# Kernel tuning notes

Hardware: AMD Instinct MI355X
Metric: run time of the kernel (lower is better)

The kernel has to match this reference:

```python
import jax, jax.numpy as jnp
import numpy as np

B, N_PER, E_PER = 100, 1000, 12000  # graphs, nodes/graph, edges/graph
N, E = B * N_PER, B * E_PER
K = int(np.ceil(0.8 * N_PER))  # TopKPooling ratio=0.8 -> 800 kept nodes/graph


def setup_inputs() -> dict:
    key = jax.random.key(0)
    ks = jax.random.split(key, 16)
    g = jnp.repeat(jnp.arange(B, dtype=jnp.int64), E_PER)
    src = g * N_PER + jax.random.randint(ks[0], (E,), 0, N_PER)
    dst = g * N_PER + jax.random.randint(ks[1], (E,), 0, N_PER)
    edge_index = jnp.stack([src, dst]).astype(jnp.int64)
    edge_attr = jax.random.uniform(ks[2], (E,), dtype=jnp.float32) + 0.1  # positive edge weights
    x = jax.random.normal(ks[3], (N, 3), dtype=jnp.float32)
    batch = jnp.repeat(jnp.arange(B, dtype=jnp.int64), N_PER)
    s = 0.1
    return {
        'x': x, 'edge_index': edge_index, 'edge_attr': edge_attr, 'batch': batch,
        'conv1_w': jax.random.normal(ks[4], (3, 64), dtype=jnp.float32) * s,
        'conv1_b': jnp.zeros((64,), dtype=jnp.float32),
        'conv2_w': jax.random.normal(ks[5], (64, 64), dtype=jnp.float32) * s,
        'conv2_b': jnp.zeros((64,), dtype=jnp.float32),
        'pool_w': jax.random.normal(ks[6], (64,), dtype=jnp.float32) * s,
        'lin1_w': jax.random.normal(ks[7], (64, 64), dtype=jnp.float32) * s,
        'lin1_b': jnp.zeros((64,), dtype=jnp.float32),
        'lin2_w': jax.random.normal(ks[8], (64, 32), dtype=jnp.float32) * s,
        'lin2_b': jnp.zeros((32,), dtype=jnp.float32),
        'lin3_w': jax.random.normal(ks[9], (32, 1), dtype=jnp.float32) * s,
        'lin3_b': jnp.zeros((1,), dtype=jnp.float32),
    }


def gcn_conv(x, row, col, ew, W, b):
    # PyG GCNConv with edge_weight and implicit self-loops (weight 1):
    # deg[i] = sum_{e: col=i} ew[e] + 1;  norm_e = d^{-1/2}[row]*ew*d^{-1/2}[col]
    h = x @ W  # [N, out]
    deg = jax.ops.segment_sum(ew, col, num_segments=N) + 1.0
    dinv = jax.lax.rsqrt(deg)
    msg = (dinv[row] * ew * dinv[col])[:, None] * h[row]  # [E, out]
    out = jax.ops.segment_sum(msg, col, num_segments=N)
    out = out + (dinv * dinv)[:, None] * h  # self-loop term
    return out + b


def reference(x, edge_index, edge_attr, batch, conv1_w, conv1_b, conv2_w, conv2_b,
              pool_w, lin1_w, lin1_b, lin2_w, lin2_b, lin3_w, lin3_b):
    row, col = edge_index[0], edge_index[1]
    h = jax.nn.relu(gcn_conv(x, row, col, edge_attr, conv1_w, conv1_b))
    x1 = h.reshape(B, N_PER, 64).mean(axis=1)  # global_mean_pool (equal-size graphs)
    h = jax.nn.relu(gcn_conv(h, row, col, edge_attr, conv2_w, conv2_b))
    # TopKPooling: score = tanh(x.w / ||w||), keep top-K per graph, gate by score
    score = jnp.tanh(h @ pool_w / jnp.linalg.norm(pool_w))  # [N]
    score_bn = score.reshape(B, N_PER)
    vals, idx = jax.lax.top_k(score_bn, K)  # [B, K]
    h_bn = h.reshape(B, N_PER, 64)
    h_sel = jnp.take_along_axis(h_bn, idx[..., None], axis=1) * vals[..., None]
    x2 = h_sel.mean(axis=1)  # global_mean_pool on pooled graph
    z = x1 + x2
    z = jax.nn.relu(z @ lin1_w + lin1_b)
    z = jax.nn.relu(z @ lin2_w + lin2_b)  # dropout is identity in eval mode
    out = jax.nn.sigmoid(z @ lin3_w + lin3_b)[:, 0]
    return out
```

## Files before the change

kernel.cpp:

```cpp
#include <hip/hip_runtime.h>

#define B_G   100
#define N_PER 1000
#define E_PER 12000
#define NTOT  (B_G * N_PER)
#define ETOT  (B_G * E_PER)
#define KSEL  800
#define EPT   12

typedef __attribute__((ext_vector_type(8))) short short8;
typedef __attribute__((ext_vector_type(4))) float float4_;

__device__ __forceinline__ unsigned short f2bf(float f) {
    unsigned u = __float_as_uint(f);
    u += 0x7fffu + ((u >> 16) & 1u);
    return (unsigned short)(u >> 16);
}
__device__ __forceinline__ float upk(unsigned q) {
    return __uint_as_float(q & 0xFFFF0000u);
}
__device__ __forceinline__ float dec_raw(unsigned byte7f) {
    return __uint_as_float(byte7f << 20);
}
__device__ __forceinline__ unsigned enc_fp8(float z) {
    unsigned u = __float_as_uint(z * 0x1p-120f);
    u += 0x7FFFFu + ((u >> 20) & 1u);
    return u >> 20;
}

#define CONV2_TI(TI, AF0, AF1) do {                                            \
    const int t_ = wid + (TI) * 16;                                            \
    const int li_ = t_ * 16 + nloc;                                            \
    const bool valid_ = li_ < N_PER;                                           \
    float acc_[16];                                                            \
    int s_ = 0, cn_ = 0;                                                       \
    if (valid_) {                                                              \
        uint4 rv_ = *(const uint4*)(zs + li_ * 64 + ((kgrp ^ ((li_ >> 1) & 3)) << 4)); \
        _Pragma("unroll")                                                      \
        for (int j = 0; j < 4; j++) {                                          \
            acc_[j]      = dec_raw((rv_.x >> (8 * j)) & 0x7Fu);                \
            acc_[4 + j]  = dec_raw((rv_.y >> (8 * j)) & 0x7Fu);                \
            acc_[8 + j]  = dec_raw((rv_.z >> (8 * j)) & 0x7Fu);                \
            acc_[12 + j] = dec_raw((rv_.w >> (8 * j)) & 0x7Fu);                \
        }                                                                      \
        s_ = li_ ? ends[li_ - 1] : 0;                                          \
        cn_ = ends[li_] - s_;                                                  \
    } else {                                                                   \
        _Pragma("unroll")                                                      \
        for (int j = 0; j < 16; j++) acc_[j] = 0.f;                            \
    }                                                                          \
    int mx_ = cn_;                                                             \
    _Pragma("unroll")                                                          \
    for (int m = 1; m < 16; m <<= 1) mx_ = max(mx_, __shfl_xor(mx_, m));       \
    for (int k = 0; k < mx_; k++) {                                            \
        if (k < cn_) {                                                         \
            unsigned q_ = csr[s_ + k];                                         \
            int src_ = (int)(q_ & 0xFFFFu);                                    \
            float wv_ = upk(q_);                                               \
            uint4 rv_ = *(const uint4*)(zs + src_ * 64 + ((kgrp ^ ((src_ >> 1) & 3)) << 4)); \
            _Pragma("unroll")                                                  \
            for (int j = 0; j < 4; j++) {                                      \
                acc_[j]      += wv_ * dec_raw((rv_.x >> (8 * j)) & 0x7Fu);     \
                acc_[4 + j]  += wv_ * dec_raw((rv_.y >> (8 * j)) & 0x7Fu);     \
                acc_[8 + j]  += wv_ * dec_raw((rv_.z >> (8 * j)) & 0x7Fu);     \
                acc_[12 + j] += wv_ * dec_raw((rv_.w >> (8 * j)) & 0x7Fu);     \
            }                                                                  \
        }                                                                      \
    }                                                                          \
    float scale_ = (valid_ ? dl[li_] : 0.f) * 0x1p120f;                        \
    _Pragma("unroll")                                                          \
    for (int j = 0; j < 8; j++) {                                              \
        AF0[j] = (short)f2bf(scale_ * acc_[j]);                                \
        AF1[j] = (short)f2bf(scale_ * acc_[8 + j]);                            \
    }                                                                          \
} while (0)

#define W2_TI(TI, AF0, AF1) do {                                               \
    const int t_ = wid + (TI) * 16;                                            \
    if (t_ < 63) {                                                             \
        float4_ accv_[4];                                                      \
        _Pragma("unroll")                                                      \
        for (int c = 0; c < 4; ++c) accv_[c] = (float4_){0.f, 0.f, 0.f, 0.f};  \
        _Pragma("unroll")                                                      \
        for (int c = 0; c < 4; ++c) {                                          \
            accv_[c] = __builtin_amdgcn_mfma_f32_16x16x32_bf16(AF0, Bf[0][c], accv_[c], 0, 0, 0); \
            accv_[c] = __builtin_amdgcn_mfma_f32_16x16x32_bf16(AF1, Bf[1][c], accv_[c], 0, 0, 0); \
        }                                                                      \
        _Pragma("unroll")                                                      \
        for (int r2 = 0; r2 < 4; ++r2) {                                       \
            int li2_ = t_ * 16 + kgrp * 4 + r2;                                \
            bool valid2_ = li2_ < N_PER;                                       \
            float sp_ = 0.f;                                                   \
            _Pragma("unroll")                                                  \
            for (int c = 0; c < 4; ++c) {                                      \
                float hv_ = fmaxf(accv_[c][r2] + b2c[c], 0.f);                 \
                sp_ += hv_ * pwc[c];                                           \
                if (valid2_) zs[li2_ * 64 + c * 16 + nloc] = (unsigned char)enc_fp8(hv_); \
            }                                                                  \
            _Pragma("unroll")                                                  \
            for (int m = 1; m < 16; m <<= 1) sp_ += __shfl_xor(sp_, m);        \
            if (valid2_ && nloc == 0) {                                        \
                float scv_ = tanhf(sp_ * invn);                                \
                unsigned bits_ = __float_as_uint(scv_);                        \
                unsigned u_ = (bits_ & 0x80000000u) ? ~bits_ : (bits_ | 0x80000000u); \
                keys[li2_] = ((unsigned long long)u_ << 32) | (unsigned)(1023 - li2_); \
            }                                                                  \
        }                                                                      \
    }                                                                          \
} while (0)

__global__ __launch_bounds__(1024)
__attribute__((amdgpu_waves_per_eu(4, 4))) void k_all(
    const int* __restrict__ ei, const float* __restrict__ ew,
    const float* __restrict__ x,
    const float* __restrict__ w1, const float* __restrict__ b1,
    const float* __restrict__ w2, const float* __restrict__ b2,
    const float* __restrict__ pw,
    const float* __restrict__ l1w, const float* __restrict__ l1b,
    const float* __restrict__ l2w, const float* __restrict__ l2b,
    const float* __restrict__ l3w, const float* __restrict__ l3b,
    float* __restrict__ out) {
    __shared__ __align__(16) unsigned char smem[136832];
    unsigned char* zs = smem;
    float* xl = (float*)smem;
    unsigned* csr = (unsigned*)(smem + 64000);
    int*   ends = (int*)(smem + 112000);
    float* dl   = (float*)(smem + 116096);
    int*   posc = (int*)(smem + 116096);
    int*   wpart = (int*)(smem + 120192);
    float* x1b   = (float*)(smem + 120192);
    unsigned char* uA = smem + 120448;
    float* aggv = (float*)uA;

    int b = blockIdx.x, tid = threadIdx.x;
    int wid = tid >> 6, lane = tid & 63;
    int gbase = b * N_PER, ebase = b * E_PER;

    int esrc[EPT], edst[EPT]; float eww[EPT];
    int ne = (tid < (E_PER - (EPT - 1) * 1024)) ? EPT : EPT - 1;
#pragma unroll
    for (int i = 0; i < EPT; i++) {
        if (i < ne) {
            int e = tid + i * 1024;
            esrc[i] = ei[ebase + e] - gbase;
            edst[i] = ei[ETOT + ebase + e] - gbase;
            eww[i]  = ew[ebase + e];
        }
    }
    ends[tid] = 0;
    for (int i = tid; i < N_PER * 3; i += 1024) xl[i] = x[(size_t)gbase * 3 + i];
    __syncthreads();
#pragma unroll
    for (int i = 0; i < EPT; i++)
        if (i < ne) atomicAdd(&ends[edst[i]], 1);
    __syncthreads();
    int v = ends[tid];
    int sc = v;
#pragma unroll
    for (int m = 1; m < 64; m <<= 1) {
        int t = __shfl_up(sc, m);
        if (lane >= m) sc += t;
    }
    if (lane == 63) wpart[wid] = sc;
    __syncthreads();
    if (tid < 16) {
        int s2 = wpart[tid];
#pragma unroll
        for (int m = 1; m < 16; m <<= 1) {
            int t = __shfl_up(s2, m);
            if (tid >= m) s2 += t;
        }
        wpart[tid] = s2;
    }
    __syncthreads();
    int incl = sc + (wid > 0 ? wpart[wid - 1] : 0);
    ends[tid] = incl;
    posc[tid] = incl - v;
    __syncthreads();
#pragma unroll
    for (int i = 0; i < EPT; i++)
        if (i < ne) {
            int p = atomicAdd(&posc[edst[i]], 1);
            csr[p] = ((unsigned)f2bf(eww[i]) << 16) | (unsigned)esrc[i];
        }
    __syncthreads();
    float dmy = 0.f;
    int s0i = 0, e0i = 0;
    if (tid < N_PER) {
        s0i = tid ? ends[tid - 1] : 0;
        e0i = ends[tid];
        float s0 = 0.f, s1 = 0.f;
        int k = s0i;
        for (; k + 2 <= e0i; k += 2) { s0 += upk(csr[k]); s1 += upk(csr[k + 1]); }
        if (k < e0i) s0 += upk(csr[k]);
        dmy = rsqrtf(s0 + s1 + 1.0f);
        dl[tid] = dmy;
        xl[tid * 3 + 0] *= dmy;
        xl[tid * 3 + 1] *= dmy;
        xl[tid * 3 + 2] *= dmy;
    }
    __syncthreads();
    if (tid < N_PER) {
        float a0 = xl[tid * 3 + 0], a1 = xl[tid * 3 + 1], a2 = xl[tid * 3 + 2];
        for (int k = s0i; k < e0i; k++) {
            unsigned q = csr[k];
            int i0 = (int)(q & 0xFFFFu) * 3;
            float wv = upk(q);
            a0 += wv * xl[i0]; a1 += wv * xl[i0 + 1]; a2 += wv * xl[i0 + 2];
        }
        aggv[tid * 3 + 0] = dmy * a0;
        aggv[tid * 3 + 1] = dmy * a1;
        aggv[tid * 3 + 2] = dmy * a2;
    }
    __syncthreads();
    {
        float w0 = w1[lane], w1v = w1[64 + lane], w2v = w1[128 + lane], bf = b1[lane];
        float* sred = (float*)(uA + 12288);
        float px = 0.f;
        int chunk = (lane & 31) >> 3;
        int word  = ((lane >= 32) ? 2 : 0) + ((lane & 7) >> 2);
        for (int node = wid; node < N_PER; node += 16) {
            float a0 = aggv[node * 3], a1 = aggv[node * 3 + 1], a2 = aggv[node * 3 + 2];
            float hv = fmaxf(a0 * w0 + a1 * w1v + a2 * w2v + bf, 0.f);
            px += hv;
            unsigned byte = enc_fp8(dl[node] * hv);
            unsigned t1 = __shfl_xor(byte, 1);
            unsigned v16 = (lane & 1) ? (t1 | (byte << 8)) : (byte | (t1 << 8));
            unsigned t2 = __shfl_xor(v16, 2);
            unsigned v32 = (lane & 2) ? (t2 | (v16 << 16)) : (v16 | (t2 << 16));
            if ((lane & 3) == 0) {
                int cs = chunk ^ ((node >> 1) & 3);
                *(unsigned*)(zs + node * 64 + cs * 16 + word * 4) = v32;
            }
        }
        sred[wid * 64 + lane] = px;
        __syncthreads();
        if (tid < 64) {
            float t = 0.f;
            for (int r = 0; r < 16; r++) t += sred[r * 64 + tid];
            x1b[tid] = t * (1.0f / N_PER);
        }
    }
    int kgrp = lane >> 4, nloc = lane & 15;
    short8 Af0a, Af0b, Af1a, Af1b, Af2a, Af2b, Af3a, Af3b;
    CONV2_TI(0, Af0a, Af0b);
    CONV2_TI(1, Af1a, Af1b);
    CONV2_TI(2, Af2a, Af2b);
    CONV2_TI(3, Af3a, Af3b);
    __syncthreads();
    unsigned long long* keys = (unsigned long long*)uA;
    {
        short8 Bf[2][4];
#pragma unroll
        for (int kh = 0; kh < 2; ++kh)
#pragma unroll
            for (int c = 0; c < 4; ++c) {
                short8 t;
#pragma unroll
                for (int j = 0; j < 8; ++j)
                    t[j] = (short)f2bf(w2[(kh * 32 + kgrp * 8 + j) * 64 + c * 16 + nloc]);
                Bf[kh][c] = t;
            }
        float b2c[4], pwc[4];
#pragma unroll
        for (int c = 0; c < 4; ++c) {
            b2c[c] = b2[c * 16 + nloc];
            pwc[c] = pw[c * 16 + nloc];
        }
        float invn;
        {
            float p = pw[lane], pn = p * p;
#pragma unroll
            for (int m = 32; m; m >>= 1) pn += __shfl_xor(pn, m);
            invn = rsqrtf(pn);
        }
        if (tid >= N_PER) keys[tid] = 0ull;
        W2_TI(0, Af0a, Af0b);
        W2_TI(1, Af1a, Af1b);
        W2_TI(2, Af2a, Af2b);
        W2_TI(3, Af3a, Af3b);
    }
    __syncthreads();
    {
        unsigned long long key = keys[tid];
        for (int k = 2; k <= 1024; k <<= 1) {
            for (int j = k >> 1; j > 0; j >>= 1) {
                bool desc = (tid & k) == 0;
                unsigned long long p;
                if (j >= 64) {
                    keys[tid] = key;
                    __syncthreads();
                    p = keys[tid ^ j];
                    __syncthreads();
                } else {
                    p = __shfl_xor(key, j);
                }
                bool low = (tid & j) == 0;
                bool sw = low ? (desc ? (key < p) : (key > p))
                              : (desc ? (p < key) : (p > key));
                if (sw) key = p;
            }
        }
        keys[tid] = key;
    }
    __syncthreads();
    float* red   = (float*)(uA + 8192);
    float* a1buf = (float*)(uA + 12288);
    float* a2buf = (float*)(uA + 12544);
    float* zbuf  = (float*)(uA + 12672);
    {
        int f = tid & 63, w16 = tid >> 6;
        float acc2 = 0.f;
        for (int r = w16; r < KSEL; r += 16) {
            unsigned long long key = keys[r];
            int idx = 1023 - (int)(key & 0xFFFFFFFFu);
            unsigned u = (unsigned)(key >> 32);
            unsigned bits = (u & 0x80000000u) ? (u & 0x7FFFFFFFu) : ~u;
            float valS = __uint_as_float(bits) * 0x1p120f;
            acc2 += valS * dec_raw((unsigned)zs[idx * 64 + f] & 0x7Fu);
        }
        red[tid] = acc2;
    }
    __syncthreads();
    if (tid < 64) {
        float s2 = 0.f;
        for (int ww = 0; ww < 16; ww++) s2 += red[ww * 64 + tid];
        zbuf[tid] = x1b[tid] + s2 * (1.0f / KSEL);
    }
    __syncthreads();
    if (tid < 64) {
        float a = l1b[tid];
        for (int k = 0; k < 64; k++) a += zbuf[k] * l1w[k * 64 + tid];
        a1buf[tid] = fmaxf(a, 0.f);
    }
    __syncthreads();
    if (tid < 32) {
        float a = l2b[tid];
        for (int k = 0; k < 64; k++) a += a1buf[k] * l2w[k * 32 + tid];
        a2buf[tid] = fmaxf(a, 0.f);
    }
    __syncthreads();
    if (tid == 0) {
        float t = l3b[0];
        for (int k = 0; k < 32; k++) t += a2buf[k] * l3w[k];
        out[b] = 1.0f / (1.0f + expf(-t));
    }
}

extern "C" void kernel_launch(void* const* d_in, const int* in_sizes, int n_in,
                              void* d_out, int out_size, void* d_ws, size_t ws_size,
                              hipStream_t stream) {
    const float* x   = (const float*)d_in[0];
    const int*   ei  = (const int*)d_in[1];
    const float* ew  = (const float*)d_in[2];
    const float* c1w = (const float*)d_in[4];
    const float* c1b = (const float*)d_in[5];
    const float* c2w = (const float*)d_in[6];
    const float* c2b = (const float*)d_in[7];
    const float* pw  = (const float*)d_in[8];
    const float* l1w = (const float*)d_in[9];
    const float* l1b = (const float*)d_in[10];
    const float* l2w = (const float*)d_in[11];
    const float* l2b = (const float*)d_in[12];
    const float* l3w = (const float*)d_in[13];
    const float* l3b = (const float*)d_in[14];
    float* out = (float*)d_out;
    (void)d_ws; (void)ws_size; (void)in_sizes; (void)n_in; (void)out_size;

    k_all<<<B_G, 1024, 0, stream>>>(ei, ew, x, c1w, c1b, c2w, c2b, pw,
                                    l1w, l1b, l2w, l2b, l3w, l3b, out);
}
```

Measured before the change: 181.3 us.

## Split each graph across two cooperating blocks with flag handoff for conv2

Launches two blocks per graph. Each block redundantly builds the CSR and runs conv1, then computes half of the conv2 row tiles. The second block copies its half of the fp8 features and score keys to workspace and sets a release flag. The first block spin-waits on that flag, copies the data back in, and runs the sort and MLP tail. This doubles the block count from 100 to 200 to fill more CUs, at the cost of duplicated front-end work, a global-memory exchange, and a spin-wait that relies on both blocks being co-resident.

```diff
diff --git a/kernel.cpp b/kernel.cpp
--- a/kernel.cpp
+++ b/kernel.cpp
@@ -109,138 +109,236 @@
     }                                                                          \
 } while (0)
 
+#define FRONT_BODY() do {                                                      \
+    int esrc[EPT], edst[EPT]; float eww[EPT];                                  \
+    int ne = (tid < (E_PER - (EPT - 1) * 1024)) ? EPT : EPT - 1;               \
+    _Pragma("unroll")                                                          \
+    for (int i = 0; i < EPT; i++) {                                            \
+        if (i < ne) {                                                          \
+            int e = tid + i * 1024;                                            \
+            esrc[i] = ei[ebase + e] - gbase;                                   \
+            edst[i] = ei[ETOT + ebase + e] - gbase;                            \
+            eww[i]  = ew[ebase + e];                                           \
+        }                                                                      \
+    }                                                                          \
+    ends[tid] = 0;                                                             \
+    for (int i = tid; i < N_PER * 3; i += 1024) xl[i] = x[(size_t)gbase * 3 + i]; \
+    __syncthreads();                                                           \
+    _Pragma("unroll")                                                          \
+    for (int i = 0; i < EPT; i++)                                              \
+        if (i < ne) atomicAdd(&ends[edst[i]], 1);                              \
+    __syncthreads();                                                           \
+    int v = ends[tid];                                                         \
+    int sc = v;                                                                \
+    _Pragma("unroll")                                                          \
+    for (int m = 1; m < 64; m <<= 1) {                                         \
+        int t = __shfl_up(sc, m);                                              \
+        if (lane >= m) sc += t;                                                \
+    }                                                                          \
+    if (lane == 63) wpart[wid] = sc;                                           \
+    __syncthreads();                                                           \
+    if (tid < 16) {                                                            \
+        int s2 = wpart[tid];                                                   \
+        _Pragma("unroll")                                                      \
+        for (int m = 1; m < 16; m <<= 1) {                                     \
+            int t = __shfl_up(s2, m);                                          \
+            if (tid >= m) s2 += t;                                             \
+        }                                                                      \
+        wpart[tid] = s2;                                                       \
+    }                                                                          \
+    __syncthreads();                                                           \
+    int incl = sc + (wid > 0 ? wpart[wid - 1] : 0);                            \
+    ends[tid] = incl;                                                          \
+    posc[tid] = incl - v;                                                      \
+    __syncthreads();                                                           \
+    _Pragma("unroll")                                                          \
+    for (int i = 0; i < EPT; i++)                                              \
+        if (i < ne) {                                                          \
+            int p = atomicAdd(&posc[edst[i]], 1);                              \
+            csr[p] = ((unsigned)f2bf(eww[i]) << 16) | (unsigned)esrc[i];       \
+        }                                                                      \
+    __syncthreads();                                                           \
+    float dmy = 0.f;                                                           \
+    int s0i = 0, e0i = 0;                                                      \
+    if (tid < N_PER) {                                                         \
+        s0i = tid ? ends[tid - 1] : 0;                                         \
+        e0i = ends[tid];                                                       \
+        float s0 = 0.f, s1 = 0.f;                                              \
+        int k = s0i;                                                           \
+        for (; k + 2 <= e0i; k += 2) { s0 += upk(csr[k]); s1 += upk(csr[k + 1]); } \
+        if (k < e0i) s0 += upk(csr[k]);                                        \
+        dmy = rsqrtf(s0 + s1 + 1.0f);                                          \
+        dl[tid] = dmy;                                                         \
+        xl[tid * 3 + 0] *= dmy;                                                \
+        xl[tid * 3 + 1] *= dmy;                                                \
+        xl[tid * 3 + 2] *= dmy;                                                \
+    }                                                                          \
+    __syncthreads();                                                           \
+    if (tid < N_PER) {                                                         \
+        float a0 = xl[tid * 3 + 0], a1 = xl[tid * 3 + 1], a2 = xl[tid * 3 + 2];\
+        for (int k = s0i; k < e0i; k++) {                                      \
+            unsigned q = csr[k];                                               \
+            int i0 = (int)(q & 0xFFFFu) * 3;                                   \
+            float wv = upk(q);                                                 \
+            a0 += wv * xl[i0]; a1 += wv * xl[i0 + 1]; a2 += wv * xl[i0 + 2];   \
+        }                                                                      \
+        aggv[tid * 3 + 0] = dmy * a0;                                          \
+        aggv[tid * 3 + 1] = dmy * a1;                                          \
+        aggv[tid * 3 + 2] = dmy * a2;                                          \
+    }                                                                          \
+    __syncthreads();                                                           \
+    {                                                                          \
+        float w0 = w1[lane], w1v = w1[64 + lane], w2v = w1[128 + lane], bf = b1[lane]; \
+        float* sred = (float*)(uA + 12288);                                    \
+        float px = 0.f;                                                        \
+        int chunk = (lane & 31) >> 3;                                          \
+        int word  = ((lane >= 32) ? 2 : 0) + ((lane & 7) >> 2);                \
+        for (int node = wid; node < N_PER; node += 16) {                       \
+            float a0 = aggv[node * 3], a1 = aggv[node * 3 + 1], a2 = aggv[node * 3 + 2]; \
+            float hv = fmaxf(a0 * w0 + a1 * w1v + a2 * w2v + bf, 0.f);         \
+            px += hv;                                                          \
+            unsigned byte = enc_fp8(dl[node] * hv);                            \
+            unsigned t1 = __shfl_xor(byte, 1);                                 \
+            unsigned v16 = (lane & 1) ? (t1 | (byte << 8)) : (byte | (t1 << 8)); \
+            unsigned t2 = __shfl_xor(v16, 2);                                  \
+            unsigned v32 = (lane & 2) ? (t2 | (v16 << 16)) : (v16 | (t2 << 16)); \
+            if ((lane & 3) == 0) {                                             \
+                int cs = chunk ^ ((node >> 1) & 3);                            \
+                *(unsigned*)(zs + node * 64 + cs * 16 + word * 4) = v32;       \
+            }                                                                  \
+        }                                                                      \
+        sred[wid * 64 + lane] = px;                                            \
+        __syncthreads();                                                       \
+        if (tid < 64) {                                                        \
+            float t = 0.f;                                                     \
+            for (int r = 0; r < 16; r++) t += sred[r * 64 + tid];              \
+            x1b[tid] = t * (1.0f / N_PER);                                     \
+        }                                                                      \
+    }                                                                          \
+} while (0)
+
+#define W2_SETUP() do {                                                        \
+    _Pragma("unroll")                                                          \
+    for (int kh = 0; kh < 2; ++kh)                                             \
+        _Pragma("unroll")                                                      \
+        for (int c = 0; c < 4; ++c) {                                          \
+            short8 t;                                                          \
+            _Pragma("unroll")                                                  \
+            for (int j = 0; j < 8; ++j)                                        \
+                t[j] = (short)f2bf(w2[(kh * 32 + kgrp * 8 + j) * 64 + c * 16 + nloc]); \
+            Bf[kh][c] = t;                                                     \
+        }                                                                      \
+    _Pragma("unroll")                                                          \
+    for (int c = 0; c < 4; ++c) {                                              \
+        b2c[c] = b2[c * 16 + nloc];                                            \
+        pwc[c] = pw[c * 16 + nloc];                                            \
+    }                                                                          \
+    {                                                                          \
+        float p = pw[lane], pn = p * p;                                        \
+        _Pragma("unroll")                                                      \
+        for (int m = 32; m; m >>= 1) pn += __shfl_xor(pn, m);                  \
+        invn = rsqrtf(pn);                                                     \
+    }                                                                          \
+} while (0)
+
+#define TAIL_BODY(OUTIDX) do {                                                 \
+    {                                                                          \
+        unsigned long long key = keys[tid];                                    \
+        for (int k = 2; k <= 1024; k <<= 1) {                                  \
+            for (int j = k >> 1; j > 0; j >>= 1) {                             \
+                bool desc = (tid & k) == 0;                                    \
+                unsigned long long p;                                          \
+                if (j >= 64) {                                                 \
+                    keys[tid] = key;                                           \
+                    __syncthreads();                                           \
+                    p = keys[tid ^ j];                                         \
+                    __syncthreads();                                           \
+                } else {                                                       \
+                    p = __shfl_xor(key, j);                                    \
+                }                                                              \
+                bool low = (tid & j) == 0;                                     \
+                bool sw = low ? (desc ? (key < p) : (key > p))                 \
+                              : (desc ? (p < key) : (p > key));                \
+                if (sw) key = p;                                               \
+            }                                                                  \
+        }                                                                      \
+        keys[tid] = key;                                                       \
+    }                                                                          \
+    __syncthreads();                                                           \
+    float* red   = (float*)(uA + 8192);                                        \
+    float* a1buf = (float*)(uA + 12288);                                       \
+    float* a2buf = (float*)(uA + 12544);                                       \
+    float* zbuf  = (float*)(uA + 12672);                                       \
+    {                                                                          \
+        int f = tid & 63, w16 = tid >> 6;                                      \
+        float acc2 = 0.f;                                                      \
+        for (int r = w16; r < KSEL; r += 16) {                                 \
+            unsigned long long key = keys[r];                                  \
+            int idx = 1023 - (int)(key & 0xFFFFFFFFu);                         \
+            unsigned u = (unsigned)(key >> 32);                                \
+            unsigned bits = (u & 0x80000000u) ? (u & 0x7FFFFFFFu) : ~u;        \
+            float valS = __uint_as_float(bits) * 0x1p120f;                     \
+            acc2 += valS * dec_raw((unsigned)zs[idx * 64 + f] & 0x7Fu);        \
+        }                                                                      \
+        red[tid] = acc2;                                                       \
+    }                                                                          \
+    __syncthreads();                                                           \
+    if (tid < 64) {                                                            \
+        float s2 = 0.f;                                                        \
+        for (int ww = 0; ww < 16; ww++) s2 += red[ww * 64 + tid];              \
+        zbuf[tid] = x1b[tid] + s2 * (1.0f / KSEL);                             \
+    }                                                                          \
+    __syncthreads();                                                           \
+    if (tid < 64) {                                                            \
+        float a = l1b[tid];                                                    \
+        for (int k = 0; k < 64; k++) a += zbuf[k] * l1w[k * 64 + tid];         \
+        a1buf[tid] = fmaxf(a, 0.f);                                            \
+    }                                                                          \
+    __syncthreads();                                                           \
+    if (tid < 32) {                                                            \
+        float a = l2b[tid];                                                    \
+        for (int k = 0; k < 64; k++) a += a1buf[k] * l2w[k * 32 + tid];        \
+        a2buf[tid] = fmaxf(a, 0.f);                                            \
+    }                                                                          \
+    __syncthreads();                                                           \
+    if (tid == 0) {                                                            \
+        float t = l3b[0];                                                      \
+        for (int k = 0; k < 32; k++) t += a2buf[k] * l3w[k];                   \
+        out[OUTIDX] = 1.0f / (1.0f + expf(-t));                                \
+    }                                                                          \
+} while (0)
+
+#define SMEM_DECLS()                                                           \
+    __shared__ __align__(16) unsigned char smem[136832];                       \
+    unsigned char* zs = smem;                                                  \
+    float* xl = (float*)smem;                                                  \
+    unsigned* csr = (unsigned*)(smem + 64000);                                 \
+    int*   ends = (int*)(smem + 112000);                                       \
+    float* dl   = (float*)(smem + 116096);                                     \
+    int*   posc = (int*)(smem + 116096);                                       \
+    int*   wpart = (int*)(smem + 120192);                                      \
+    float* x1b   = (float*)(smem + 120192);                                    \
+    unsigned char* uA = smem + 120448;                                         \
+    float* aggv = (float*)uA;
+
+#define PARAMS                                                                 \
+    const int* __restrict__ ei, const float* __restrict__ ew,                  \
+    const float* __restrict__ x,                                               \
+    const float* __restrict__ w1, const float* __restrict__ b1,                \
+    const float* __restrict__ w2, const float* __restrict__ b2,                \
+    const float* __restrict__ pw,                                              \
+    const float* __restrict__ l1w, const float* __restrict__ l1b,              \
+    const float* __restrict__ l2w, const float* __restrict__ l2b,              \
+    const float* __restrict__ l3w, const float* __restrict__ l3b,              \
+    float* __restrict__ out
+
 __global__ __launch_bounds__(1024)
-__attribute__((amdgpu_waves_per_eu(4, 4))) void k_all(
-    const int* __restrict__ ei, const float* __restrict__ ew,
-    const float* __restrict__ x,
-    const float* __restrict__ w1, const float* __restrict__ b1,
-    const float* __restrict__ w2, const float* __restrict__ b2,
-    const float* __restrict__ pw,
-    const float* __restrict__ l1w, const float* __restrict__ l1b,
-    const float* __restrict__ l2w, const float* __restrict__ l2b,
-    const float* __restrict__ l3w, const float* __restrict__ l3b,
-    float* __restrict__ out) {
-    __shared__ __align__(16) unsigned char smem[136832];
-    unsigned char* zs = smem;
-    float* xl = (float*)smem;
-    unsigned* csr = (unsigned*)(smem + 64000);
-    int*   ends = (int*)(smem + 112000);
-    float* dl   = (float*)(smem + 116096);
-    int*   posc = (int*)(smem + 116096);
-    int*   wpart = (int*)(smem + 120192);
-    float* x1b   = (float*)(smem + 120192);
-    unsigned char* uA = smem + 120448;
-    float* aggv = (float*)uA;
-
-    int b = blockIdx.x, tid = threadIdx.x;
+__attribute__((amdgpu_waves_per_eu(4, 4))) void k_all_single(PARAMS) {
+    SMEM_DECLS();
+    int g = blockIdx.x, tid = threadIdx.x;
     int wid = tid >> 6, lane = tid & 63;
-    int gbase = b * N_PER, ebase = b * E_PER;
-
-    int esrc[EPT], edst[EPT]; float eww[EPT];
-    int ne = (tid < (E_PER - (EPT - 1) * 1024)) ? EPT : EPT - 1;
-#pragma unroll
-    for (int i = 0; i < EPT; i++) {
-        if (i < ne) {
-            int e = tid + i * 1024;
-            esrc[i] = ei[ebase + e] - gbase;
-            edst[i] = ei[ETOT + ebase + e] - gbase;
-            eww[i]  = ew[ebase + e];
-        }
-    }
-    ends[tid] = 0;
-    for (int i = tid; i < N_PER * 3; i += 1024) xl[i] = x[(size_t)gbase * 3 + i];
-    __syncthreads();
-#pragma unroll
-    for (int i = 0; i < EPT; i++)
-        if (i < ne) atomicAdd(&ends[edst[i]], 1);
-    __syncthreads();
-    int v = ends[tid];
-    int sc = v;
-#pragma unroll
-    for (int m = 1; m < 64; m <<= 1) {
-        int t = __shfl_up(sc, m);
-        if (lane >= m) sc += t;
-    }
-    if (lane == 63) wpart[wid] = sc;
-    __syncthreads();
-    if (tid < 16) {
-        int s2 = wpart[tid];
-#pragma unroll
-        for (int m = 1; m < 16; m <<= 1) {
-            int t = __shfl_up(s2, m);
-            if (tid >= m) s2 += t;
-        }
-        wpart[tid] = s2;
-    }
-    __syncthreads();
-    int incl = sc + (wid > 0 ? wpart[wid - 1] : 0);
-    ends[tid] = incl;
-    posc[tid] = incl - v;
-    __syncthreads();
-#pragma unroll
-    for (int i = 0; i < EPT; i++)
-        if (i < ne) {
-            int p = atomicAdd(&posc[edst[i]], 1);
-            csr[p] = ((unsigned)f2bf(eww[i]) << 16) | (unsigned)esrc[i];
-        }
-    __syncthreads();
-    float dmy = 0.f;
-    int s0i = 0, e0i = 0;
-    if (tid < N_PER) {
-        s0i = tid ? ends[tid - 1] : 0;
-        e0i = ends[tid];
-        float s0 = 0.f, s1 = 0.f;
-        int k = s0i;
-        for (; k + 2 <= e0i; k += 2) { s0 += upk(csr[k]); s1 += upk(csr[k + 1]); }
-        if (k < e0i) s0 += upk(csr[k]);
-        dmy = rsqrtf(s0 + s1 + 1.0f);
-        dl[tid] = dmy;
-        xl[tid * 3 + 0] *= dmy;
-        xl[tid * 3 + 1] *= dmy;
-        xl[tid * 3 + 2] *= dmy;
-    }
-    __syncthreads();
-    if (tid < N_PER) {
-        float a0 = xl[tid * 3 + 0], a1 = xl[tid * 3 + 1], a2 = xl[tid * 3 + 2];
-        for (int k = s0i; k < e0i; k++) {
-            unsigned q = csr[k];
-            int i0 = (int)(q & 0xFFFFu) * 3;
-            float wv = upk(q);
-            a0 += wv * xl[i0]; a1 += wv * xl[i0 + 1]; a2 += wv * xl[i0 + 2];
-        }
-        aggv[tid * 3 + 0] = dmy * a0;
-        aggv[tid * 3 + 1] = dmy * a1;
-        aggv[tid * 3 + 2] = dmy * a2;
-    }
-    __syncthreads();
-    {
-        float w0 = w1[lane], w1v = w1[64 + lane], w2v = w1[128 + lane], bf = b1[lane];
-        float* sred = (float*)(uA + 12288);
-        float px = 0.f;
-        int chunk = (lane & 31) >> 3;
-        int word  = ((lane >= 32) ? 2 : 0) + ((lane & 7) >> 2);
-        for (int node = wid; node < N_PER; node += 16) {
-            float a0 = aggv[node * 3], a1 = aggv[node * 3 + 1], a2 = aggv[node * 3 + 2];
-            float hv = fmaxf(a0 * w0 + a1 * w1v + a2 * w2v + bf, 0.f);
-            px += hv;
-            unsigned byte = enc_fp8(dl[node] * hv);
-            unsigned t1 = __shfl_xor(byte, 1);
-            unsigned v16 = (lane & 1) ? (t1 | (byte << 8)) : (byte | (t1 << 8));
-            unsigned t2 = __shfl_xor(v16, 2);
-            unsigned v32 = (lane & 2) ? (t2 | (v16 << 16)) : (v16 | (t2 << 16));
-            if ((lane & 3) == 0) {
-                int cs = chunk ^ ((node >> 1) & 3);
-                *(unsigned*)(zs + node * 64 + cs * 16 + word * 4) = v32;
-            }
-        }
-        sred[wid * 64 + lane] = px;
-        __syncthreads();
-        if (tid < 64) {
-            float t = 0.f;
-            for (int r = 0; r < 16; r++) t += sred[r * 64 + tid];
-            x1b[tid] = t * (1.0f / N_PER);
-        }
-    }
+    int gbase = g * N_PER, ebase = g * E_PER;
+    FRONT_BODY();
     int kgrp = lane >> 4, nloc = lane & 15;
     short8 Af0a, Af0b, Af1a, Af1b, Af2a, Af2b, Af3a, Af3b;
     CONV2_TI(0, Af0a, Af0b);
@@ -250,30 +348,8 @@
     __syncthreads();
     unsigned long long* keys = (unsigned long long*)uA;
     {
-        short8 Bf[2][4];
-#pragma unroll
-        for (int kh = 0; kh < 2; ++kh)
-#pragma unroll
-            for (int c = 0; c < 4; ++c) {
-                short8 t;
-#pragma unroll
-                for (int j = 0; j < 8; ++j)
-                    t[j] = (short)f2bf(w2[(kh * 32 + kgrp * 8 + j) * 64 + c * 16 + nloc]);
-                Bf[kh][c] = t;
-            }
-        float b2c[4], pwc[4];
-#pragma unroll
-        for (int c = 0; c < 4; ++c) {
-            b2c[c] = b2[c * 16 + nloc];
-            pwc[c] = pw[c * 16 + nloc];
-        }
-        float invn;
-        {
-            float p = pw[lane], pn = p * p;
-#pragma unroll
-            for (int m = 32; m; m >>= 1) pn += __shfl_xor(pn, m);
-            invn = rsqrtf(pn);
-        }
+        short8 Bf[2][4]; float b2c[4], pwc[4], invn;
+        W2_SETUP();
         if (tid >= N_PER) keys[tid] = 0ull;
         W2_TI(0, Af0a, Af0b);
         W2_TI(1, Af1a, Af1b);
@@ -281,70 +357,64 @@
         W2_TI(3, Af3a, Af3b);
     }
     __syncthreads();
+    TAIL_BODY(g);
+}
+
+__global__ __launch_bounds__(1024)
+__attribute__((amdgpu_waves_per_eu(4, 4))) void k_all_pair(
+    PARAMS, unsigned char* __restrict__ ws) {
+    SMEM_DECLS();
+    int g = blockIdx.x >> 1, half = blockIdx.x & 1, tid = threadIdx.x;
+    int wid = tid >> 6, lane = tid & 63;
+    int gbase = g * N_PER, ebase = g * E_PER;
+    unsigned int* flag = (unsigned int*)ws;
+    unsigned char* h2x = ws + 4096 + (size_t)g * 32768;
+    unsigned long long* kx =
+        (unsigned long long*)(ws + 4096 + 100 * 32768 + (size_t)g * 4096);
+
+    FRONT_BODY();
+    int kgrp = lane >> 4, nloc = lane & 15;
+    const int tiA = half * 2, tiB = half * 2 + 1;
+    short8 AfAa, AfAb, AfBa, AfBb;
+    CONV2_TI(tiA, AfAa, AfAb);
+    CONV2_TI(tiB, AfBa, AfBb);
+    __syncthreads();
+    unsigned long long* keys = (unsigned long long*)uA;
     {
-        unsigned long long key = keys[tid];
-        for (int k = 2; k <= 1024; k <<= 1) {
-            for (int j = k >> 1; j > 0; j >>= 1) {
-                bool desc = (tid & k) == 0;
-                unsigned long long p;
-                if (j >= 64) {
-                    keys[tid] = key;
-                    __syncthreads();
-                    p = keys[tid ^ j];
-                    __syncthreads();
-                } else {
-                    p = __shfl_xor(key, j);
-                }
-                bool low = (tid & j) == 0;
-                bool sw = low ? (desc ? (key < p) : (key > p))
-                              : (desc ? (p < key) : (p > key));
-                if (sw) key = p;
-            }
+        short8 Bf[2][4]; float b2c[4], pwc[4], invn;
+        W2_SETUP();
+        if (tid >= N_PER) keys[tid] = 0ull;
+        W2_TI(tiA, AfAa, AfAb);
+        W2_TI(tiB, AfBa, AfBb);
+    }
+    __syncthreads();
+    if (half) {
+        const uint4* srcv = (const uint4*)(zs + 32768);
+        uint4* dstv = (uint4*)h2x;
+        for (int i = tid; i < 1952; i += 1024) dstv[i] = srcv[i];
+        for (int i = tid; i < 512; i += 1024) kx[i] = keys[512 + i];
+        __syncthreads();
+        if (tid == 0)
+            __hip_atomic_store(flag + g, 1u, __ATOMIC_RELEASE,
+                               __HIP_MEMORY_SCOPE_AGENT);
+        return;
+    }
+    if (tid == 0) {
+        for (int it = 0; it < 1000000; ++it) {
+            if (__hip_atomic_load(flag + g, __ATOMIC_ACQUIRE,
+                                  __HIP_MEMORY_SCOPE_AGENT) != 0u) break;
+            __builtin_amdgcn_s_sleep(8);
         }
-        keys[tid] = key;
-    }
-    __syncthreads();
-    float* red   = (float*)(uA + 8192);
-    float* a1buf = (float*)(uA + 12288);
-    float* a2buf = (float*)(uA + 12544);
-    float* zbuf  = (float*)(uA + 12672);
+    }
+    __syncthreads();
     {
-        int f = tid & 63, w16 = tid >> 6;
-        float acc2 = 0.f;
-        for (int r = w16; r < KSEL; r += 16) {
-            unsigned long long key = keys[r];
-            int idx = 1023 - (int)(key & 0xFFFFFFFFu);
-            unsigned u = (unsigned)(key >> 32);
-            unsigned bits = (u & 0x80000000u) ? (u & 0x7FFFFFFFu) : ~u;
-            float valS = __uint_as_float(bits) * 0x1p120f;
-            acc2 += valS * dec_raw((unsigned)zs[idx * 64 + f] & 0x7Fu);
-        }
-        red[tid] = acc2;
-    }
-    __syncthreads();
-    if (tid < 64) {
-        float s2 = 0.f;
-        for (int ww = 0; ww < 16; ww++) s2 += red[ww * 64 + tid];
-        zbuf[tid] = x1b[tid] + s2 * (1.0f / KSEL);
-    }
-    __syncthreads();
-    if (tid < 64) {
-        float a = l1b[tid];
-        for (int k = 0; k < 64; k++) a += zbuf[k] * l1w[k * 64 + tid];
-        a1buf[tid] = fmaxf(a, 0.f);
-    }
-    __syncthreads();
-    if (tid < 32) {
-        float a = l2b[tid];
-        for (int k = 0; k < 64; k++) a += a1buf[k] * l2w[k * 32 + tid];
-        a2buf[tid] = fmaxf(a, 0.f);
-    }
-    __syncthreads();
-    if (tid == 0) {
-        float t = l3b[0];
-        for (int k = 0; k < 32; k++) t += a2buf[k] * l3w[k];
-        out[b] = 1.0f / (1.0f + expf(-t));
-    }
+        uint4* dstv = (uint4*)(zs + 32768);
+        const uint4* srcv = (const uint4*)h2x;
+        for (int i = tid; i < 1952; i += 1024) dstv[i] = srcv[i];
+        for (int i = tid; i < 512; i += 1024) keys[512 + i] = kx[i];
+    }
+    __syncthreads();
+    TAIL_BODY(g);
 }
 
 extern "C" void kernel_launch(void* const* d_in, const int* in_sizes, int n_in,
@@ -365,8 +435,17 @@
     const float* l3w = (const float*)d_in[13];
     const float* l3b = (const float*)d_in[14];
     float* out = (float*)d_out;
-    (void)d_ws; (void)ws_size; (void)in_sizes; (void)n_in; (void)out_size;
-
-    k_all<<<B_G, 1024, 0, stream>>>(ei, ew, x, c1w, c1b, c2w, c2b, pw,
-                                    l1w, l1b, l2w, l2b, l3w, l3b, out);
-}
+    (void)in_sizes; (void)n_in; (void)out_size;
+
+    const size_t needed = 4096 + (size_t)100 * 32768 + (size_t)100 * 4096;
+    if (d_ws != nullptr && ws_size >= needed) {
+        hipMemsetAsync(d_ws, 0, 512, stream);
+        k_all_pair<<<2 * B_G, 1024, 0, stream>>>(
+            ei, ew, x, c1w, c1b, c2w, c2b, pw,
+            l1w, l1b, l2w, l2b, l3w, l3b, out, (unsigned char*)d_ws);
+    } else {
+        k_all_single<<<B_G, 1024, 0, stream>>>(
+            ei, ew, x, c1w, c1b, c2w, c2b, pw,
+            l1w, l1b, l2w, l2b, l3w, l3b, out);
+    }
+}
```

Measured after the change: 171.3 us. 1.06x faster.
